# Performance work log

Hardware: AMD Instinct MI355X
Metric: run time of the kernel (lower is better)

Reference implementation:

```python
import jax, jax.numpy as jnp
import numpy as np

B = 64        # number of graphs in the batch
NPG = 1024    # nodes per graph (uniform batch_num_nodes)
N = B * NPG   # total nodes = 65536
D = 512       # input feature dim
DEG = 32      # average degree
K = 0.5       # keep-percent
DROP = NPG - int(np.ceil(K * NPG))  # number of lowest-score nodes zeroed per graph


def setup_inputs() -> dict:
    key = jax.random.key(0)
    k1, k2, k3, k4 = jax.random.split(key, 4)
    features = jax.random.normal(k1, (N, D), dtype=jnp.float32)
    # edges constrained inside each graph's node block (batched DGL graph is block-diagonal)
    offsets = (jnp.arange(B, dtype=jnp.int64) * NPG)[:, None]
    src = (jax.random.randint(k2, (B, NPG * DEG), 0, NPG, dtype=jnp.int64) + offsets).reshape(-1)
    dst = (jax.random.randint(k3, (B, NPG * DEG), 0, NPG, dtype=jnp.int64) + offsets).reshape(-1)
    # GraphConv(input_dim=D, out=1) parameters (glorot-ish scale)
    weight = jax.random.normal(k4, (D, 1), dtype=jnp.float32) * (1.0 / np.sqrt(D))
    bias = jnp.zeros((1,), dtype=jnp.float32)
    return {"features": features, "src": src, "dst": dst, "weight": weight, "bias": bias}


def reference(features, src, dst, weight, bias):
    # --- GraphConv(D -> 1, norm=True, bias=True, activation=relu) ---
    # old-DGL norm=True: symmetric normalization with in-degrees, norm=deg^-0.5 (0 for isolated)
    deg = jnp.zeros((N,), features.dtype).at[dst].add(1.0)
    norm = jnp.where(deg > 0, deg ** -0.5, 0.0)[:, None]          # [N,1]
    # in_feats > out_feats: project first, then aggregate scalars
    h = (features @ weight) * norm                                # [N,1]
    agg = jnp.zeros_like(h).at[dst].add(h[src])                   # sum over in-edges
    w = jax.nn.relu(agg * norm + bias)                            # [N,1] scores
    # --- per-graph top-k masking: zero the DROP smallest scores in each graph ---
    wb = w.reshape(B, NPG)
    ranks = jnp.argsort(jnp.argsort(wb, axis=1), axis=1)          # rank 0 = smallest
    wb = jnp.where(ranks < DROP, jnp.zeros((), wb.dtype), wb)
    # --- elementwise gating of features by (masked) scores ---
    return features * wb.reshape(N, 1)
```

## Files before the change

kernel.cpp:

```cpp
#include <hip/hip_runtime.h>

#define NTOT 65536
#define DIM  512
#define BGR  64
#define NPG  1024
#define DROPN 512

__global__ void matvec_kernel(const float* __restrict__ X,
                              const float* __restrict__ W,
                              float* __restrict__ p) {
    int gid  = blockIdx.x * blockDim.x + threadIdx.x;
    int row  = gid >> 6;
    int lane = gid & 63;
    if (row >= NTOT) return;
    const float4* xr = (const float4*)(X + (size_t)row * DIM);
    const float4* wr = (const float4*)W;
    float4 a0 = xr[lane];
    float4 a1 = xr[lane + 64];
    float4 w0 = wr[lane];
    float4 w1 = wr[lane + 64];
    float s = a0.x*w0.x + a0.y*w0.y + a0.z*w0.z + a0.w*w0.w
            + a1.x*w1.x + a1.y*w1.y + a1.z*w1.z + a1.w*w1.w;
    #pragma unroll
    for (int off = 32; off > 0; off >>= 1)
        s += __shfl_down(s, off, 64);
    if (lane == 0) p[row] = s;
}

__global__ __launch_bounds__(1024) void fused_graph_kernel(
        const int* __restrict__ src, const int* __restrict__ dst,
        const float* __restrict__ p, const float* __restrict__ bias,
        float* __restrict__ gate, int epg) {
    __shared__ float degs[NPG];
    __shared__ float hn[NPG];
    __shared__ float agg[NPG];
    __shared__ unsigned long long keys[NPG];

    const int g = blockIdx.x;
    const int t = threadIdx.x;
    const int nbase = g * NPG;

    degs[t] = 0.f;
    agg[t]  = 0.f;
    __syncthreads();

    const int4* dst4 = (const int4*)(dst + (size_t)g * epg);
    const int4* src4 = (const int4*)(src + (size_t)g * epg);
    const int n4 = epg >> 2;
    for (int i = t; i < n4; i += 1024) {
        int4 d = dst4[i];
        atomicAdd(&degs[d.x - nbase], 1.f);
        atomicAdd(&degs[d.y - nbase], 1.f);
        atomicAdd(&degs[d.z - nbase], 1.f);
        atomicAdd(&degs[d.w - nbase], 1.f);
    }
    __syncthreads();

    const float d   = degs[t];
    const float nrm = d > 0.f ? (1.0f / sqrtf(d)) : 0.f;
    hn[t] = p[nbase + t] * nrm;
    __syncthreads();

    for (int i = t; i < n4; i += 1024) {
        int4 s = src4[i];
        int4 d2 = dst4[i];
        atomicAdd(&agg[d2.x - nbase], hn[s.x - nbase]);
        atomicAdd(&agg[d2.y - nbase], hn[s.y - nbase]);
        atomicAdd(&agg[d2.z - nbase], hn[s.z - nbase]);
        atomicAdd(&agg[d2.w - nbase], hn[s.w - nbase]);
    }
    __syncthreads();

    float w = agg[t] * nrm + bias[0];
    w = w > 0.f ? w : 0.f;
    hn[t] = w;
    keys[t] = ((unsigned long long)__float_as_uint(w) << 32) | (unsigned int)t;
    __syncthreads();

    for (int k = 2; k <= NPG; k <<= 1) {
        for (int j = k >> 1; j > 0; j >>= 1) {
            int ixj = t ^ j;
            if (ixj > t) {
                unsigned long long a = keys[t], c = keys[ixj];
                bool up = ((t & k) == 0);
                if ((a > c) == up) { keys[t] = c; keys[ixj] = a; }
            }
            __syncthreads();
        }
    }

    int idx = (int)(keys[t] & 0xffffffffull);
    gate[nbase + idx] = (t < DROPN) ? 0.f : hn[idx];
}

__global__ void gate_kernel(const float* __restrict__ X,
                            const float* __restrict__ gate,
                            float* __restrict__ out) {
    int gid  = blockIdx.x * blockDim.x + threadIdx.x;
    int row  = gid >> 6;
    int lane = gid & 63;
    if (row >= NTOT) return;
    float g = gate[row];
    float4* orow = (float4*)(out + (size_t)row * DIM);
    if (g == 0.f) {
        float4 z = make_float4(0.f, 0.f, 0.f, 0.f);
        orow[lane] = z;
        orow[lane + 64] = z;
    } else {
        const float4* xr = (const float4*)(X + (size_t)row * DIM);
        float4 a = xr[lane], c = xr[lane + 64];
        a.x *= g; a.y *= g; a.z *= g; a.w *= g;
        c.x *= g; c.y *= g; c.z *= g; c.w *= g;
        orow[lane] = a;
        orow[lane + 64] = c;
    }
}

extern "C" void kernel_launch(void* const* d_in, const int* in_sizes, int n_in,
                              void* d_out, int out_size, void* d_ws, size_t ws_size,
                              hipStream_t stream) {
    const float* X    = (const float*)d_in[0];
    const int*   src  = (const int*)d_in[1];
    const int*   dst  = (const int*)d_in[2];
    const float* W    = (const float*)d_in[3];
    const float* bias = (const float*)d_in[4];
    float* out = (float*)d_out;
    int E   = in_sizes[1];
    int epg = E / BGR;

    float* ws   = (float*)d_ws;
    float* p    = ws;
    float* gate = ws + NTOT;

    matvec_kernel<<<NTOT / 4, 256, 0, stream>>>(X, W, p);
    fused_graph_kernel<<<BGR, 1024, 0, stream>>>(src, dst, p, bias, gate, epg);
    gate_kernel<<<NTOT / 4, 256, 0, stream>>>(X, gate, out);
}
```

Before: 339.4 us.

## Split graph conv edge passes across slices with global atomics; persistent matvec/gate

Splits the single per-graph fused kernel, which used only 64 blocks, into separate degree, normalize, aggregate and top-k kernels. Each graph's edge list is divided into 8 slices, giving 512 blocks that accumulate in shared memory and merge through global atomics. The matvec and gate kernels become grid-stride loops, matvec processes two rows per iteration, and gate uses nontemporal stores. The cost is extra launches, a memset, and global atomic traffic in exchange for more parallelism in the edge phases. Float atomic merge order can also change aggregation rounding.

New measurement: 284.9 us. 1.19x faster.

```diff
diff --git a/kernel.cpp b/kernel.cpp
--- a/kernel.cpp
+++ b/kernel.cpp
@@ -5,78 +5,120 @@
 #define BGR  64
 #define NPG  1024
 #define DROPN 512
+#define SLICES 8
 
-__global__ void matvec_kernel(const float* __restrict__ X,
-                              const float* __restrict__ W,
-                              float* __restrict__ p) {
-    int gid  = blockIdx.x * blockDim.x + threadIdx.x;
-    int row  = gid >> 6;
-    int lane = gid & 63;
-    if (row >= NTOT) return;
-    const float4* xr = (const float4*)(X + (size_t)row * DIM);
-    const float4* wr = (const float4*)W;
-    float4 a0 = xr[lane];
-    float4 a1 = xr[lane + 64];
-    float4 w0 = wr[lane];
-    float4 w1 = wr[lane + 64];
-    float s = a0.x*w0.x + a0.y*w0.y + a0.z*w0.z + a0.w*w0.w
-            + a1.x*w1.x + a1.y*w1.y + a1.z*w1.z + a1.w*w1.w;
-    #pragma unroll
-    for (int off = 32; off > 0; off >>= 1)
-        s += __shfl_down(s, off, 64);
-    if (lane == 0) p[row] = s;
+typedef float vf4 __attribute__((ext_vector_type(4)));
+
+__global__ __launch_bounds__(256) void matvec_kernel(
+        const float* __restrict__ X, const float* __restrict__ W,
+        float* __restrict__ p) {
+    const int lane = threadIdx.x & 63;
+    const int nw   = (gridDim.x * blockDim.x) >> 6;
+    const int wid  = (blockIdx.x * blockDim.x + threadIdx.x) >> 6;
+    const vf4* wr = (const vf4*)W;
+    const vf4 w0 = wr[lane], w1 = wr[lane + 64];
+    for (int row = wid; row < NTOT; row += 2 * nw) {
+        const int row2 = row + nw;
+        const vf4* xr0 = (const vf4*)(X + (size_t)row  * DIM);
+        const vf4* xr1 = (const vf4*)(X + (size_t)row2 * DIM);
+        vf4 a0 = xr0[lane], a1 = xr0[lane + 64];
+        vf4 b0 = xr1[lane], b1 = xr1[lane + 64];
+        vf4 m0 = a0 * w0 + a1 * w1;
+        vf4 m1 = b0 * w0 + b1 * w1;
+        float s0 = m0[0] + m0[1] + m0[2] + m0[3];
+        float s1 = m1[0] + m1[1] + m1[2] + m1[3];
+        #pragma unroll
+        for (int off = 32; off > 0; off >>= 1) {
+            s0 += __shfl_down(s0, off, 64);
+            s1 += __shfl_down(s1, off, 64);
+        }
+        if (lane == 0) { p[row] = s0; p[row2] = s1; }
+    }
 }
 
-__global__ __launch_bounds__(1024) void fused_graph_kernel(
+__global__ __launch_bounds__(256) void deg_partial_kernel(
+        const int* __restrict__ dst, float* __restrict__ deg, int epg) {
+    __shared__ int dl[NPG];
+    const int g = blockIdx.x & (BGR - 1);
+    const int slice = blockIdx.x >> 6;
+    const int nbase = g * NPG;
+    const int eps = epg / SLICES;
+    for (int i = threadIdx.x; i < NPG; i += 256) dl[i] = 0;
+    __syncthreads();
+    const int4* d4 = (const int4*)(dst + (size_t)g * epg + (size_t)slice * eps);
+    const int n4 = eps >> 2;
+    for (int i = threadIdx.x; i < n4; i += 256) {
+        int4 d = d4[i];
+        atomicAdd(&dl[d.x - nbase], 1);
+        atomicAdd(&dl[d.y - nbase], 1);
+        atomicAdd(&dl[d.z - nbase], 1);
+        atomicAdd(&dl[d.w - nbase], 1);
+    }
+    __syncthreads();
+    for (int i = threadIdx.x; i < NPG; i += 256) {
+        int c = dl[i];
+        if (c) atomicAdd(&deg[nbase + i], (float)c);
+    }
+}
+
+__global__ __launch_bounds__(256) void hn_kernel(
+        const float* __restrict__ p, const float* __restrict__ deg,
+        float* __restrict__ hn) {
+    int i = blockIdx.x * blockDim.x + threadIdx.x;
+    if (i < NTOT) {
+        float d = deg[i];
+        float nrm = d > 0.f ? (1.0f / sqrtf(d)) : 0.f;
+        hn[i] = p[i] * nrm;
+    }
+}
+
+__global__ __launch_bounds__(256) void agg_partial_kernel(
         const int* __restrict__ src, const int* __restrict__ dst,
-        const float* __restrict__ p, const float* __restrict__ bias,
-        float* __restrict__ gate, int epg) {
-    __shared__ float degs[NPG];
-    __shared__ float hn[NPG];
-    __shared__ float agg[NPG];
+        const float* __restrict__ hn, float* __restrict__ agg, int epg) {
+    __shared__ float al[NPG];
+    __shared__ float hl[NPG];
+    const int g = blockIdx.x & (BGR - 1);
+    const int slice = blockIdx.x >> 6;
+    const int nbase = g * NPG;
+    const int eps = epg / SLICES;
+    for (int i = threadIdx.x; i < NPG; i += 256) {
+        al[i] = 0.f;
+        hl[i] = hn[nbase + i];
+    }
+    __syncthreads();
+    const int4* s4 = (const int4*)(src + (size_t)g * epg + (size_t)slice * eps);
+    const int4* d4 = (const int4*)(dst + (size_t)g * epg + (size_t)slice * eps);
+    const int n4 = eps >> 2;
+    for (int i = threadIdx.x; i < n4; i += 256) {
+        int4 s = s4[i];
+        int4 d = d4[i];
+        atomicAdd(&al[d.x - nbase], hl[s.x - nbase]);
+        atomicAdd(&al[d.y - nbase], hl[s.y - nbase]);
+        atomicAdd(&al[d.z - nbase], hl[s.z - nbase]);
+        atomicAdd(&al[d.w - nbase], hl[s.w - nbase]);
+    }
+    __syncthreads();
+    for (int i = threadIdx.x; i < NPG; i += 256) {
+        float v = al[i];
+        if (v != 0.f) atomicAdd(&agg[nbase + i], v);
+    }
+}
+
+__global__ __launch_bounds__(1024) void topk_kernel(
+        const float* __restrict__ agg, const float* __restrict__ deg,
+        const float* __restrict__ bias, float* __restrict__ gate) {
     __shared__ unsigned long long keys[NPG];
-
+    __shared__ float wv[NPG];
     const int g = blockIdx.x;
     const int t = threadIdx.x;
     const int nbase = g * NPG;
-
-    degs[t] = 0.f;
-    agg[t]  = 0.f;
-    __syncthreads();
-
-    const int4* dst4 = (const int4*)(dst + (size_t)g * epg);
-    const int4* src4 = (const int4*)(src + (size_t)g * epg);
-    const int n4 = epg >> 2;
-    for (int i = t; i < n4; i += 1024) {
-        int4 d = dst4[i];
-        atomicAdd(&degs[d.x - nbase], 1.f);
-        atomicAdd(&degs[d.y - nbase], 1.f);
-        atomicAdd(&degs[d.z - nbase], 1.f);
-        atomicAdd(&degs[d.w - nbase], 1.f);
-    }
-    __syncthreads();
-
-    const float d   = degs[t];
-    const float nrm = d > 0.f ? (1.0f / sqrtf(d)) : 0.f;
-    hn[t] = p[nbase + t] * nrm;
-    __syncthreads();
-
-    for (int i = t; i < n4; i += 1024) {
-        int4 s = src4[i];
-        int4 d2 = dst4[i];
-        atomicAdd(&agg[d2.x - nbase], hn[s.x - nbase]);
-        atomicAdd(&agg[d2.y - nbase], hn[s.y - nbase]);
-        atomicAdd(&agg[d2.z - nbase], hn[s.z - nbase]);
-        atomicAdd(&agg[d2.w - nbase], hn[s.w - nbase]);
-    }
-    __syncthreads();
-
-    float w = agg[t] * nrm + bias[0];
+    float d = deg[nbase + t];
+    float nrm = d > 0.f ? (1.0f / sqrtf(d)) : 0.f;
+    float w = agg[nbase + t] * nrm + bias[0];
     w = w > 0.f ? w : 0.f;
-    hn[t] = w;
+    wv[t] = w;
     keys[t] = ((unsigned long long)__float_as_uint(w) << 32) | (unsigned int)t;
     __syncthreads();
-
     for (int k = 2; k <= NPG; k <<= 1) {
         for (int j = k >> 1; j > 0; j >>= 1) {
             int ixj = t ^ j;
@@ -88,31 +130,30 @@
             __syncthreads();
         }
     }
-
     int idx = (int)(keys[t] & 0xffffffffull);
-    gate[nbase + idx] = (t < DROPN) ? 0.f : hn[idx];
+    gate[nbase + idx] = (t < DROPN) ? 0.f : wv[idx];
 }
 
-__global__ void gate_kernel(const float* __restrict__ X,
-                            const float* __restrict__ gate,
-                            float* __restrict__ out) {
-    int gid  = blockIdx.x * blockDim.x + threadIdx.x;
-    int row  = gid >> 6;
-    int lane = gid & 63;
-    if (row >= NTOT) return;
-    float g = gate[row];
-    float4* orow = (float4*)(out + (size_t)row * DIM);
-    if (g == 0.f) {
-        float4 z = make_float4(0.f, 0.f, 0.f, 0.f);
-        orow[lane] = z;
-        orow[lane + 64] = z;
-    } else {
-        const float4* xr = (const float4*)(X + (size_t)row * DIM);
-        float4 a = xr[lane], c = xr[lane + 64];
-        a.x *= g; a.y *= g; a.z *= g; a.w *= g;
-        c.x *= g; c.y *= g; c.z *= g; c.w *= g;
-        orow[lane] = a;
-        orow[lane + 64] = c;
+__global__ __launch_bounds__(256) void gate_kernel(
+        const float* __restrict__ X, const float* __restrict__ gate,
+        float* __restrict__ out) {
+    const int lane = threadIdx.x & 63;
+    const int nw   = (gridDim.x * blockDim.x) >> 6;
+    const int wid  = (blockIdx.x * blockDim.x + threadIdx.x) >> 6;
+    for (int row = wid; row < NTOT; row += nw) {
+        float g = gate[__builtin_amdgcn_readfirstlane(row)];
+        vf4* o = (vf4*)(out + (size_t)row * DIM);
+        if (g == 0.f) {
+            vf4 z = (vf4){0.f, 0.f, 0.f, 0.f};
+            __builtin_nontemporal_store(z, &o[lane]);
+            __builtin_nontemporal_store(z, &o[lane + 64]);
+        } else {
+            const vf4* xr = (const vf4*)(X + (size_t)row * DIM);
+            vf4 a = xr[lane] * g;
+            vf4 c = xr[lane + 64] * g;
+            __builtin_nontemporal_store(a, &o[lane]);
+            __builtin_nontemporal_store(c, &o[lane + 64]);
+        }
     }
 }
 
@@ -130,9 +171,17 @@
 
     float* ws   = (float*)d_ws;
     float* p    = ws;
-    float* gate = ws + NTOT;
+    float* hn   = ws + 1 * NTOT;
+    float* deg  = ws + 2 * NTOT;
+    float* agg  = ws + 3 * NTOT;
+    float* gate = ws + 4 * NTOT;
 
-    matvec_kernel<<<NTOT / 4, 256, 0, stream>>>(X, W, p);
-    fused_graph_kernel<<<BGR, 1024, 0, stream>>>(src, dst, p, bias, gate, epg);
-    gate_kernel<<<NTOT / 4, 256, 0, stream>>>(X, gate, out);
+    hipMemsetAsync(deg, 0, 2 * NTOT * sizeof(float), stream);
+
+    matvec_kernel<<<2048, 256, 0, stream>>>(X, W, p);
+    deg_partial_kernel<<<BGR * SLICES, 256, 0, stream>>>(dst, deg, epg);
+    hn_kernel<<<NTOT / 256, 256, 0, stream>>>(p, deg, hn);
+    agg_partial_kernel<<<BGR * SLICES, 256, 0, stream>>>(src, dst, hn, agg, epg);
+    topk_kernel<<<BGR, 1024, 0, stream>>>(agg, deg, bias, gate);
+    gate_kernel<<<2048, 256, 0, stream>>>(X, gate, out);
 }
```
